# Performance work log

Measured on AMD Instinct MI355X. Metric: run time of the kernel, lower is better.

## Reference

```python
import jax, jax.numpy as jnp
import numpy as np


def _maxpool2(x):
    # x: [B, C, H, W] -> [B, C, H//2, W//2], 2x2 max pool stride 2
    B, C, H, W = x.shape
    return x.reshape(B, C, H // 2, 2, W // 2, 2).max(axis=(3, 5))


def setup_inputs() -> dict:
    key = jax.random.key(0)
    ks = jax.random.split(key, 6)
    B, C, H, W = 16, 128, 64, 64
    x = jax.random.normal(ks[0], (B, C, H, W), dtype=jnp.float32)
    wq = jax.random.normal(ks[1], (C // 8, C), dtype=jnp.float32) * 0.05
    wk = jax.random.normal(ks[2], (C // 8, C), dtype=jnp.float32) * 0.05
    wv = jax.random.normal(ks[3], (C // 2, C), dtype=jnp.float32) * 0.05
    wo = jax.random.normal(ks[4], (C, C // 2), dtype=jnp.float32) * 0.05
    gamma = jax.random.uniform(ks[5], (1,), dtype=jnp.float32)
    return {"x": x, "wq": wq, "wk": wk, "wv": wv, "wo": wo, "gamma": gamma}


def reference(x, wq, wk, wv, wo, gamma):
    B, C, H, W = x.shape
    N = H * W
    M = N // 4
    # 1x1 convs are channel contractions
    q = jnp.einsum('oc,bchw->bohw', wq, x)              # [B, C/8, H, W]
    k = _maxpool2(jnp.einsum('oc,bchw->bohw', wk, x))   # [B, C/8, H/2, W/2]
    v = _maxpool2(jnp.einsum('oc,bchw->bohw', wv, x))   # [B, C/2, H/2, W/2]
    q = q.reshape(B, C // 8, N)
    k = k.reshape(B, C // 8, M)
    v = v.reshape(B, C // 2, M)
    attn = jax.nn.softmax(jnp.einsum('bcn,bcm->bnm', q, k), axis=-1)  # [B, N, M]
    o = jnp.einsum('bcm,bnm->bcn', v, attn).reshape(B, C // 2, H, W)
    o = jnp.einsum('oc,bchw->bohw', wo, o)              # [B, C, H, W]
    return gamma[0] * o + x
```

## Files before the change

### kernel.cpp

```cpp
#include <hip/hip_runtime.h>


#define LOG2E 1.4426950408889634f

typedef __attribute__((ext_vector_type(8)))  short bf16x8;
typedef __attribute__((ext_vector_type(16))) float f32x16;
typedef unsigned long long ull;

static __device__ __forceinline__ unsigned cvt_pk_bf16(float a, float b) {
  unsigned r;
  asm("v_cvt_pk_bf16_f32 %0, %1, %2" : "=v"(r) : "v"(a), "v"(b));
  return r;
}
static __device__ __forceinline__ void perm32swap(unsigned& a, unsigned& b) {
  asm volatile("v_permlane32_swap_b32 %0, %1" : "+v"(a), "+v"(b));
}
static __device__ __forceinline__ float fexp2(float x) {
  float r; asm("v_exp_f32 %0, %1" : "=v"(r) : "v"(x)); return r;
}
static __device__ __forceinline__ bf16x8 pack4(unsigned u0, unsigned u1,
                                               unsigned u2, unsigned u3) {
  union { bf16x8 v; unsigned u[4]; } r;
  r.u[0] = u0; r.u[1] = u1; r.u[2] = u2; r.u[3] = u3;
  return r.v;
}
static __device__ __forceinline__ bf16x8 pack2ull(ull a, ull b) {
  union { bf16x8 v; ull u[2]; } r;
  r.u[0] = a; r.u[1] = b;
  return r.v;
}
static __device__ __forceinline__ short f2bf(float f) {
  unsigned u = __float_as_uint(f);
  u = (u + 0x7FFFu + ((u >> 16) & 1u)) >> 16;
  return (short)u;
}

#define WSTRIDE 136

__global__ __launch_bounds__(256) void proj_kernel(
    const float* __restrict__ x, const float* __restrict__ wq,
    const float* __restrict__ wk, const float* __restrict__ wv,
    short* __restrict__ qT, short* __restrict__ kT, short* __restrict__ vO)
{
  __shared__ short w_s[96 * WSTRIDE];
  __shared__ short v_s[64 * 32];

  const int b = blockIdx.y, t = threadIdx.x;
  const int wid = t >> 6, lane = t & 63;
  const int l31 = lane & 31, hi = lane >> 5;
  const int p = blockIdx.x * 128 + wid * 32 + l31;
  const int q2 = p >> 2, rr = p & 3;
  const int nsp = ((((q2 >> 5) << 1) | (rr >> 1)) << 6) | (((q2 & 31) << 1) | (rr & 1));

  const float* xc = x + (size_t)b * 128 * 4096 + (size_t)hi * 8 * 4096 + nsp;
  float xv[8][8];
  #pragma unroll
  for (int cc = 0; cc < 8; ++cc)
    #pragma unroll
    for (int j = 0; j < 8; ++j)
      xv[cc][j] = xc[(size_t)(cc * 16 + j) * 4096];

  #pragma unroll
  for (int kk = 0; kk < 12; ++kk) {
    const int idx = t + kk * 256;
    const int row = idx >> 5, c4 = (idx & 31) << 2;
    const float* src = (row < 16) ? (wq + row * 128 + c4)
                     : (row < 32) ? (wk + (row - 16) * 128 + c4)
                                  : (wv + (row - 32) * 128 + c4);
    const float4 f = *(const float4*)src;
    const ull v = ((ull)cvt_pk_bf16(f.z, f.w) << 32) | (ull)cvt_pk_bf16(f.x, f.y);
    *(ull*)&w_s[row * WSTRIDE + c4] = v;
  }
  __syncthreads();

  bf16x8 xf[8];
  #pragma unroll
  for (int cc = 0; cc < 8; ++cc)
    xf[cc] = pack4(cvt_pk_bf16(xv[cc][0], xv[cc][1]), cvt_pk_bf16(xv[cc][2], xv[cc][3]),
                   cvt_pk_bf16(xv[cc][4], xv[cc][5]), cvt_pk_bf16(xv[cc][6], xv[cc][7]));

  f32x16 acc0, acc1, acc2;
  #pragma unroll
  for (int j = 0; j < 16; ++j) { acc0[j] = 0.f; acc1[j] = 0.f; acc2[j] = 0.f; }

  #pragma unroll
  for (int cc = 0; cc < 8; ++cc) {
    const int off = cc * 16 + hi * 8;
    const bf16x8 a0 = *(const bf16x8*)&w_s[l31 * WSTRIDE + off];
    const bf16x8 a1 = *(const bf16x8*)&w_s[(32 + l31) * WSTRIDE + off];
    const bf16x8 a2 = *(const bf16x8*)&w_s[(64 + l31) * WSTRIDE + off];
    acc0 = __builtin_amdgcn_mfma_f32_32x32x16_bf16(a0, xf[cc], acc0, 0, 0, 0);
    acc1 = __builtin_amdgcn_mfma_f32_32x32x16_bf16(a1, xf[cc], acc1, 0, 0, 0);
    acc2 = __builtin_amdgcn_mfma_f32_32x32x16_bf16(a2, xf[cc], acc2, 0, 0, 0);
  }

  {
    unsigned u0 = cvt_pk_bf16(acc0[0] * LOG2E, acc0[1] * LOG2E);
    unsigned u1 = cvt_pk_bf16(acc0[2] * LOG2E, acc0[3] * LOG2E);
    unsigned u2 = cvt_pk_bf16(acc0[4] * LOG2E, acc0[5] * LOG2E);
    unsigned u3 = cvt_pk_bf16(acc0[6] * LOG2E, acc0[7] * LOG2E);
    perm32swap(u0, u2); perm32swap(u1, u3);
    *(bf16x8*)(qT + ((size_t)b * 4096 + p) * 16 + hi * 8) = pack4(u0, u1, u2, u3);
  }

  {
    float pk[8];
    #pragma unroll
    for (int r = 8; r < 16; ++r) {
      float m = acc0[r];
      m = fmaxf(m, __shfl_xor(m, 1));
      m = fmaxf(m, __shfl_xor(m, 2));
      pk[r - 8] = m;
    }
    unsigned u0 = cvt_pk_bf16(pk[0], pk[1]), u1 = cvt_pk_bf16(pk[2], pk[3]);
    unsigned u2 = cvt_pk_bf16(pk[4], pk[5]), u3 = cvt_pk_bf16(pk[6], pk[7]);
    perm32swap(u0, u2); perm32swap(u1, u3);
    if ((l31 & 3) == 0)
      *(bf16x8*)(kT + ((size_t)b * 1024 + (p >> 2)) * 16 + hi * 8) =
          pack4(u0, u1, u2, u3);
  }

  {
    float pv1[16], pv2[16];
    #pragma unroll
    for (int r = 0; r < 16; ++r) {
      float m1 = acc1[r], m2 = acc2[r];
      m1 = fmaxf(m1, __shfl_xor(m1, 1)); m1 = fmaxf(m1, __shfl_xor(m1, 2));
      m2 = fmaxf(m2, __shfl_xor(m2, 1)); m2 = fmaxf(m2, __shfl_xor(m2, 2));
      pv1[r] = m1; pv2[r] = m2;
    }
    if ((l31 & 3) == 0) {
      const int q2l = wid * 8 + (l31 >> 2);
      #pragma unroll
      for (int r = 0; r < 16; ++r) {
        const int c2 = (r & 3) + 8 * (r >> 2) + 4 * hi;
        v_s[c2 * 32 + q2l]        = f2bf(pv1[r]);
        v_s[(32 + c2) * 32 + q2l] = f2bf(pv2[r]);
      }
    }
  }
  __syncthreads();
  {
    const int c2 = t >> 2, off = (t & 3) * 8;
    *(bf16x8*)(vO + ((size_t)b * 64 + c2) * 1024 + blockIdx.x * 32 + off) =
        *(const bf16x8*)&v_s[c2 * 32 + off];
  }
}

#define WOSTRIDE 68

__global__ __launch_bounds__(256) void attn_kernel(
    const short* __restrict__ qT, const short* __restrict__ kT,
    const short* __restrict__ vO, const float* __restrict__ wo,
    const float* __restrict__ x, const float* __restrict__ gamma,
    float* __restrict__ out)
{
  __shared__ short wo_s[128 * WOSTRIDE];

  const int t = threadIdx.x;
  const int wid = t >> 6, lane = t & 63;
  const int l31 = lane & 31, hi = lane >> 5;

  const int wg = blockIdx.x;
  const int swz = (wg & 7) * 64 + (wg >> 3);
  const int b = swz >> 5;
  const int p = (swz & 31) * 128 + wid * 32 + l31;

  #pragma unroll
  for (int kk = 0; kk < 8; ++kk) {
    const int idx = t + kk * 256;
    const int row = idx >> 4, c4 = (idx & 15) << 2;
    const float4 f = *(const float4*)(wo + row * 64 + c4);
    const ull v = ((ull)cvt_pk_bf16(f.z, f.w) << 32) | (ull)cvt_pk_bf16(f.x, f.y);
    *(ull*)&wo_s[row * WOSTRIDE + c4] = v;
  }

  const short* kTb = kT + (size_t)b * 1024 * 16;
  const short* vb  = vO + (size_t)b * 64 * 1024;
  const bf16x8 qf = *(const bf16x8*)(qT + ((size_t)b * 4096 + p) * 16 + hi * 8);

  f32x16 z, o0, o1;
  #pragma unroll
  for (int j = 0; j < 16; ++j) { z[j] = 0.f; o0[j] = 0.f; o1[j] = 0.f; }
  float l = 0.f;

  bf16x8 kfA, v00A, v01A, v10A, v11A;
  bf16x8 kfB, v00B, v01B, v10B, v11B;

#define LOADT(S, M0) do {                                                    \
    const int m0_ = (M0);                                                    \
    kf##S  = *(const bf16x8*)(kTb + (size_t)(m0_ + l31) * 16 + hi * 8);      \
    const size_t r0_ = (size_t)l31 * 1024 + m0_ + hi * 8;                    \
    v00##S = *(const bf16x8*)(vb + r0_);                                     \
    v01##S = *(const bf16x8*)(vb + r0_ + 16);                                \
    v10##S = *(const bf16x8*)(vb + r0_ + 32 * 1024);                         \
    v11##S = *(const bf16x8*)(vb + r0_ + 32 * 1024 + 16); } while (0)

#define COMP(S) do {                                                         \
    f32x16 s = __builtin_amdgcn_mfma_f32_32x32x16_bf16(kf##S, qf, z, 0, 0, 0);\
    float pe[16];                                                            \
    _Pragma("unroll")                                                        \
    for (int j = 0; j < 16; ++j) pe[j] = fexp2(s[j]);                        \
    l += ((pe[0]+pe[1])+(pe[2]+pe[3])) + ((pe[4]+pe[5])+(pe[6]+pe[7]))       \
       + ((pe[8]+pe[9])+(pe[10]+pe[11])) + ((pe[12]+pe[13])+(pe[14]+pe[15]));\
    unsigned a0 = cvt_pk_bf16(pe[0], pe[1]),  a1 = cvt_pk_bf16(pe[2], pe[3]);\
    unsigned a2 = cvt_pk_bf16(pe[4], pe[5]),  a3 = cvt_pk_bf16(pe[6], pe[7]);\
    perm32swap(a0, a2); perm32swap(a1, a3);                                  \
    const bf16x8 P0 = pack4(a0, a1, a2, a3);                                 \
    unsigned c0 = cvt_pk_bf16(pe[8], pe[9]),   c1 = cvt_pk_bf16(pe[10], pe[11]);\
    unsigned c2 = cvt_pk_bf16(pe[12], pe[13]), c3 = cvt_pk_bf16(pe[14], pe[15]);\
    perm32swap(c0, c2); perm32swap(c1, c3);                                  \
    const bf16x8 P1 = pack4(c0, c1, c2, c3);                                 \
    o0 = __builtin_amdgcn_mfma_f32_32x32x16_bf16(v00##S, P0, o0, 0, 0, 0);   \
    o0 = __builtin_amdgcn_mfma_f32_32x32x16_bf16(v01##S, P1, o0, 0, 0, 0);   \
    o1 = __builtin_amdgcn_mfma_f32_32x32x16_bf16(v10##S, P0, o1, 0, 0, 0);   \
    o1 = __builtin_amdgcn_mfma_f32_32x32x16_bf16(v11##S, P1, o1, 0, 0, 0); } while (0)

  LOADT(A, 0);
  #pragma unroll 1
  for (int mt = 0; mt < 32; mt += 2) {
    LOADT(B, (mt + 1) * 32);
    __builtin_amdgcn_s_setprio(1);
    COMP(A);
    __builtin_amdgcn_s_setprio(0);
    const int mn = (mt + 2 < 32) ? (mt + 2) * 32 : 0;
    LOADT(A, mn);
    __builtin_amdgcn_s_setprio(1);
    COMP(B);
    __builtin_amdgcn_s_setprio(0);
  }
#undef LOADT
#undef COMP

  __syncthreads();

  l += __shfl_xor(l, 32);
  const float inv = 1.0f / l;

  float on[32];
  #pragma unroll
  for (int j = 0; j < 16; ++j) { on[j] = o0[j] * inv; on[16 + j] = o1[j] * inv; }

  bf16x8 ofr[4];
  #pragma unroll
  for (int ck = 0; ck < 4; ++ck) {
    const int base = (ck >> 1) * 16 + (ck & 1) * 8;
    unsigned a0 = cvt_pk_bf16(on[base + 0], on[base + 1]);
    unsigned a1 = cvt_pk_bf16(on[base + 2], on[base + 3]);
    unsigned a2 = cvt_pk_bf16(on[base + 4], on[base + 5]);
    unsigned a3 = cvt_pk_bf16(on[base + 6], on[base + 7]);
    perm32swap(a0, a2); perm32swap(a1, a3);
    ofr[ck] = pack4(a0, a1, a2, a3);
  }

  const int q2 = p >> 2, rr = p & 3;
  const int nsp = ((((q2 >> 5) << 1) | (rr >> 1)) << 6) | (((q2 & 31) << 1) | (rr & 1));
  const float g = gamma[0];
  const float* xb = x + (size_t)b * 128 * 4096 + nsp;
  float* ob = out + (size_t)b * 128 * 4096 + nsp;

  #pragma unroll 1
  for (int cot = 0; cot < 4; ++cot) {
    f32x16 acc;
    #pragma unroll
    for (int j = 0; j < 16; ++j) acc[j] = 0.f;
    #pragma unroll
    for (int ck = 0; ck < 4; ++ck) {
      const short* pw = &wo_s[(cot * 32 + l31) * WOSTRIDE + ck * 16 + hi * 8];
      const bf16x8 wf = pack2ull(*(const ull*)pw, *(const ull*)(pw + 4));
      acc = __builtin_amdgcn_mfma_f32_32x32x16_bf16(wf, ofr[ck], acc, 0, 0, 0);
    }
    #pragma unroll
    for (int r = 0; r < 16; ++r) {
      const int co = cot * 32 + (r & 3) + 8 * (r >> 2) + 4 * hi;
      ob[(size_t)co * 4096] = g * acc[r] + xb[(size_t)co * 4096];
    }
  }
}

extern "C" void kernel_launch(void* const* d_in, const int* in_sizes, int n_in,
                              void* d_out, int out_size, void* d_ws, size_t ws_size,
                              hipStream_t stream) {
  const float* x     = (const float*)d_in[0];
  const float* wq    = (const float*)d_in[1];
  const float* wk    = (const float*)d_in[2];
  const float* wv    = (const float*)d_in[3];
  const float* wo    = (const float*)d_in[4];
  const float* gamma = (const float*)d_in[5];
  float* out = (float*)d_out;

  short* ws = (short*)d_ws;
  short* qT = ws;
  short* kT = ws + 1048576;
  short* vO = ws + 1310720;

  proj_kernel<<<dim3(32, 16), 256, 0, stream>>>(x, wq, wk, wv, qT, kT, vO);
  attn_kernel<<<dim3(512), 256, 0, stream>>>(qT, kT, vO, wo, x, gamma, out);
}
```

Baseline: 137.9 us.

## Split attention keys across wave pairs and stage x through swizzled LDS

The attention kernel now gives each workgroup 64 queries instead of 128 and splits the 1024 keys between two waves per query tile, doubling the grid to 1024 blocks. Partial outputs and softmax denominators are combined through shared memory, and each wave of the pair then handles half of the output-channel projection. This raises occupancy and parallelism at the cost of extra LDS traffic and barriers. Separately, the projection kernel loads x with coalesced float4 row reads into a swizzled bf16 LDS tile instead of strided scalar gathers.

```diff
diff --git a/kernel.cpp b/kernel.cpp
--- a/kernel.cpp
+++ b/kernel.cpp
@@ -34,6 +34,10 @@
   u = (u + 0x7FFFu + ((u >> 16) & 1u)) >> 16;
   return (short)u;
 }
+static __device__ __forceinline__ int swzj(int j) {
+  return j ^ ((j >> 2) & 7) ^ (((j >> 6) & 1) << 2);
+}
+#define FK(V, K) ((K) == 0 ? (V).x : (K) == 1 ? (V).y : (K) == 2 ? (V).z : (V).w)
 
 #define WSTRIDE 136
 
@@ -42,23 +46,35 @@
     const float* __restrict__ wk, const float* __restrict__ wv,
     short* __restrict__ qT, short* __restrict__ kT, short* __restrict__ vO)
 {
+  __shared__ short x_s[16 * 1024];
   __shared__ short w_s[96 * WSTRIDE];
   __shared__ short v_s[64 * 32];
 
   const int b = blockIdx.y, t = threadIdx.x;
   const int wid = t >> 6, lane = t & 63;
   const int l31 = lane & 31, hi = lane >> 5;
-  const int p = blockIdx.x * 128 + wid * 32 + l31;
-  const int q2 = p >> 2, rr = p & 3;
-  const int nsp = ((((q2 >> 5) << 1) | (rr >> 1)) << 6) | (((q2 & 31) << 1) | (rr & 1));
-
-  const float* xc = x + (size_t)b * 128 * 4096 + (size_t)hi * 8 * 4096 + nsp;
-  float xv[8][8];
-  #pragma unroll
-  for (int cc = 0; cc < 8; ++cc)
-    #pragma unroll
-    for (int j = 0; j < 8; ++j)
-      xv[cc][j] = xc[(size_t)(cc * 16 + j) * 4096];
+  const int r = blockIdx.x;
+  const float* xb = x + (size_t)b * 128 * 4096 + r * 128;
+
+  const int j4  = (t & 31) * 4;
+  const int c00 = (t >> 5) * 8;
+  #pragma unroll
+  for (int R = 0; R < 2; ++R) {
+    float4 f[8];
+    #pragma unroll
+    for (int i = 0; i < 8; ++i)
+      f[i] = *(const float4*)(xb + (size_t)(c00 + i + R * 64) * 4096 + j4);
+    const int g = (t >> 5) + R * 8;
+    #pragma unroll
+    for (int k = 0; k < 4; ++k) {
+      const bf16x8 frag = pack4(
+          cvt_pk_bf16(FK(f[0], k), FK(f[1], k)),
+          cvt_pk_bf16(FK(f[2], k), FK(f[3], k)),
+          cvt_pk_bf16(FK(f[4], k), FK(f[5], k)),
+          cvt_pk_bf16(FK(f[6], k), FK(f[7], k)));
+      *(bf16x8*)&x_s[g * 1024 + swzj(j4 + k) * 8] = frag;
+    }
+  }
 
   #pragma unroll
   for (int kk = 0; kk < 12; ++kk) {
@@ -73,11 +89,15 @@
   }
   __syncthreads();
 
+  const int p_local = wid * 32 + l31;
+  const int q2l = p_local >> 2, rr = p_local & 3;
+  const int jl = (rr >> 1) * 64 + q2l * 2 + (rr & 1);
+  const int p = r * 128 + p_local;
+
   bf16x8 xf[8];
   #pragma unroll
   for (int cc = 0; cc < 8; ++cc)
-    xf[cc] = pack4(cvt_pk_bf16(xv[cc][0], xv[cc][1]), cvt_pk_bf16(xv[cc][2], xv[cc][3]),
-                   cvt_pk_bf16(xv[cc][4], xv[cc][5]), cvt_pk_bf16(xv[cc][6], xv[cc][7]));
+    xf[cc] = *(const bf16x8*)&x_s[(cc * 2 + hi) * 1024 + swzj(jl) * 8];
 
   f32x16 acc0, acc1, acc2;
   #pragma unroll
@@ -106,11 +126,11 @@
   {
     float pk[8];
     #pragma unroll
-    for (int r = 8; r < 16; ++r) {
-      float m = acc0[r];
+    for (int rg = 8; rg < 16; ++rg) {
+      float m = acc0[rg];
       m = fmaxf(m, __shfl_xor(m, 1));
       m = fmaxf(m, __shfl_xor(m, 2));
-      pk[r - 8] = m;
+      pk[rg - 8] = m;
     }
     unsigned u0 = cvt_pk_bf16(pk[0], pk[1]), u1 = cvt_pk_bf16(pk[2], pk[3]);
     unsigned u2 = cvt_pk_bf16(pk[4], pk[5]), u3 = cvt_pk_bf16(pk[6], pk[7]);
@@ -123,26 +143,26 @@
   {
     float pv1[16], pv2[16];
     #pragma unroll
-    for (int r = 0; r < 16; ++r) {
-      float m1 = acc1[r], m2 = acc2[r];
+    for (int rg = 0; rg < 16; ++rg) {
+      float m1 = acc1[rg], m2 = acc2[rg];
       m1 = fmaxf(m1, __shfl_xor(m1, 1)); m1 = fmaxf(m1, __shfl_xor(m1, 2));
       m2 = fmaxf(m2, __shfl_xor(m2, 1)); m2 = fmaxf(m2, __shfl_xor(m2, 2));
-      pv1[r] = m1; pv2[r] = m2;
+      pv1[rg] = m1; pv2[rg] = m2;
     }
     if ((l31 & 3) == 0) {
-      const int q2l = wid * 8 + (l31 >> 2);
+      const int q2p = wid * 8 + (l31 >> 2);
       #pragma unroll
-      for (int r = 0; r < 16; ++r) {
-        const int c2 = (r & 3) + 8 * (r >> 2) + 4 * hi;
-        v_s[c2 * 32 + q2l]        = f2bf(pv1[r]);
-        v_s[(32 + c2) * 32 + q2l] = f2bf(pv2[r]);
+      for (int rg = 0; rg < 16; ++rg) {
+        const int c2 = (rg & 3) + 8 * (rg >> 2) + 4 * hi;
+        v_s[c2 * 32 + q2p]        = f2bf(pv1[rg]);
+        v_s[(32 + c2) * 32 + q2p] = f2bf(pv2[rg]);
       }
     }
   }
   __syncthreads();
   {
     const int c2 = t >> 2, off = (t & 3) * 8;
-    *(bf16x8*)(vO + ((size_t)b * 64 + c2) * 1024 + blockIdx.x * 32 + off) =
+    *(bf16x8*)(vO + ((size_t)b * 64 + c2) * 1024 + r * 32 + off) =
         *(const bf16x8*)&v_s[c2 * 32 + off];
   }
 }
@@ -155,16 +175,19 @@
     const float* __restrict__ x, const float* __restrict__ gamma,
     float* __restrict__ out)
 {
+  __shared__ float obuf[2][2][64][18];
+  __shared__ float lbuf[2][2][64];
   __shared__ short wo_s[128 * WOSTRIDE];
 
   const int t = threadIdx.x;
   const int wid = t >> 6, lane = t & 63;
   const int l31 = lane & 31, hi = lane >> 5;
+  const int qhalf = wid >> 1, mhalf = wid & 1;
 
   const int wg = blockIdx.x;
-  const int swz = (wg & 7) * 64 + (wg >> 3);
-  const int b = swz >> 5;
-  const int p = (swz & 31) * 128 + wid * 32 + l31;
+  const int sw = (wg & 7) * 128 + (wg >> 3);
+  const int b = sw >> 6;
+  const int p = (sw & 63) * 64 + qhalf * 32 + l31;
 
   #pragma unroll
   for (int kk = 0; kk < 8; ++kk) {
@@ -183,6 +206,8 @@
   #pragma unroll
   for (int j = 0; j < 16; ++j) { z[j] = 0.f; o0[j] = 0.f; o1[j] = 0.f; }
   float l = 0.f;
+
+  const int mbase = mhalf * 512;
 
   bf16x8 kfA, v00A, v01A, v10A, v11A;
   bf16x8 kfB, v00B, v01B, v10B, v11B;
@@ -216,14 +241,14 @@
     o1 = __builtin_amdgcn_mfma_f32_32x32x16_bf16(v10##S, P0, o1, 0, 0, 0);   \
     o1 = __builtin_amdgcn_mfma_f32_32x32x16_bf16(v11##S, P1, o1, 0, 0, 0); } while (0)
 
-  LOADT(A, 0);
+  LOADT(A, mbase);
   #pragma unroll 1
-  for (int mt = 0; mt < 32; mt += 2) {
-    LOADT(B, (mt + 1) * 32);
+  for (int mt = 0; mt < 16; mt += 2) {
+    LOADT(B, mbase + (mt + 1) * 32);
     __builtin_amdgcn_s_setprio(1);
     COMP(A);
     __builtin_amdgcn_s_setprio(0);
-    const int mn = (mt + 2 < 32) ? (mt + 2) * 32 : 0;
+    const int mn = (mt + 2 < 16) ? mbase + (mt + 2) * 32 : mbase;
     LOADT(A, mn);
     __builtin_amdgcn_s_setprio(1);
     COMP(B);
@@ -232,9 +257,24 @@
 #undef LOADT
 #undef COMP
 
-  __syncthreads();
-
   l += __shfl_xor(l, 32);
+  float* mybuf = &obuf[qhalf][mhalf][lane][0];
+  const float* pbuf = &obuf[qhalf][mhalf ^ 1][lane][0];
+
+  #pragma unroll
+  for (int j = 0; j < 16; ++j) mybuf[j] = o0[j];
+  lbuf[qhalf][mhalf][lane] = l;
+  __syncthreads();
+  #pragma unroll
+  for (int j = 0; j < 16; ++j) o0[j] += pbuf[j];
+  l += lbuf[qhalf][mhalf ^ 1][lane];
+  __syncthreads();
+  #pragma unroll
+  for (int j = 0; j < 16; ++j) mybuf[j] = o1[j];
+  __syncthreads();
+  #pragma unroll
+  for (int j = 0; j < 16; ++j) o1[j] += pbuf[j];
+
   const float inv = 1.0f / l;
 
   float on[32];
@@ -260,7 +300,8 @@
   float* ob = out + (size_t)b * 128 * 4096 + nsp;
 
   #pragma unroll 1
-  for (int cot = 0; cot < 4; ++cot) {
+  for (int ci = 0; ci < 2; ++ci) {
+    const int cot = mhalf * 2 + ci;
     f32x16 acc;
     #pragma unroll
     for (int j = 0; j < 16; ++j) acc[j] = 0.f;
@@ -271,9 +312,9 @@
       acc = __builtin_amdgcn_mfma_f32_32x32x16_bf16(wf, ofr[ck], acc, 0, 0, 0);
     }
     #pragma unroll
-    for (int r = 0; r < 16; ++r) {
-      const int co = cot * 32 + (r & 3) + 8 * (r >> 2) + 4 * hi;
-      ob[(size_t)co * 4096] = g * acc[r] + xb[(size_t)co * 4096];
+    for (int rg = 0; rg < 16; ++rg) {
+      const int co = cot * 32 + (rg & 3) + 8 * (rg >> 2) + 4 * hi;
+      ob[(size_t)co * 4096] = g * acc[rg] + xb[(size_t)co * 4096];
     }
   }
 }
@@ -295,5 +336,5 @@
   short* vO = ws + 1310720;
 
   proj_kernel<<<dim3(32, 16), 256, 0, stream>>>(x, wq, wk, wv, qT, kT, vO);
-  attn_kernel<<<dim3(512), 256, 0, stream>>>(qT, kT, vO, wo, x, gamma, out);
-}
+  attn_kernel<<<dim3(1024), 256, 0, stream>>>(qT, kT, vO, wo, x, gamma, out);
+}
```

After: 135.2 us. 2.0% less time.
